# Optimization experiments

Hardware: AMD Instinct MI355X
Metric: run time of the kernel (lower is better)

## Reference

```python
import jax, jax.numpy as jnp
import numpy as np

EPS = 1e-5

def _bin_act(x):
    # sign() forward, clipped straight-through estimator backward
    xc = jnp.clip(x, -1.0, 1.0)
    return xc + jax.lax.stop_gradient(jnp.sign(x) - xc)

def _bin_w(w):
    # XNOR-style: sign(w) scaled by per-output-channel mean(|w|); identity STE
    alpha = jnp.mean(jnp.abs(w), axis=(1, 2, 3), keepdims=True)
    return w + jax.lax.stop_gradient(jnp.sign(w) * alpha - w)

def _conv(x, w, stride, padding, groups):
    return jax.lax.conv_general_dilated(
        x, w, window_strides=(stride, stride),
        padding=[(padding, padding), (padding, padding)],
        feature_group_count=groups,
        dimension_numbers=('NCHW', 'OIHW', 'NCHW'))

def _binconv(x, w, stride, padding, groups):
    return _conv(_bin_act(x), _bin_w(w), stride, padding, groups)

def _bn(x, g, b, m, v):
    # eval-mode BatchNorm2d
    inv = g / jnp.sqrt(v + EPS)
    return x * inv[None, :, None, None] + (b - m * inv)[None, :, None, None]


def setup_inputs() -> dict:
    key = jax.random.key(0)
    ks = jax.random.split(key, 20)
    inp, oup = 256, 512
    d = {}
    d['x'] = jax.random.normal(ks[0], (64, inp, 28, 28), jnp.float32)
    d['w1'] = jax.random.normal(ks[1], (inp, 16, 3, 3), jnp.float32) * 0.1  # grouped, groups=inp/16
    d['w2'] = jax.random.normal(ks[2], (oup, inp, 1, 1), jnp.float32) * 0.05
    d['w3'] = jax.random.normal(ks[3], (oup, oup, 1, 1), jnp.float32) * 0.05
    for i, (name, c) in enumerate([('1', inp), ('2', oup), ('3', oup)]):
        d['g' + name] = jax.random.uniform(ks[4 + 4 * i], (c,), jnp.float32, 0.5, 1.5)
        d['b' + name] = jax.random.normal(ks[5 + 4 * i], (c,), jnp.float32) * 0.1
        d['m' + name] = jax.random.normal(ks[6 + 4 * i], (c,), jnp.float32) * 0.1
        d['v' + name] = jax.random.uniform(ks[7 + 4 * i], (c,), jnp.float32, 0.5, 1.5)
    return d


def reference(x, w1, w2, w3, g1, b1, m1, v1, g2, b2, m2, v2, g3, b3, m3, v3):
    inp = x.shape[1]
    groups = inp // 16
    # conv1 (binary grouped 3x3) + bn1 + residual + hardtanh
    out = _bn(_binconv(x, w1, 1, 1, groups), g1, b1, m1, v1)
    out = jnp.clip(out + x, -1.0, 1.0)
    # conv2 (binary 1x1, inp->oup) + bn2 + hardtanh
    out = jnp.clip(_bn(_binconv(out, w2, 1, 0, 1), g2, b2, m2, v2), -1.0, 1.0)
    res = out
    # conv3 (binary 1x1, oup->oup) + bn3 + residual + hardtanh
    out = _bn(_binconv(out, w3, 1, 0, 1), g3, b3, m3, v3)
    return jnp.clip(out + res, -1.0, 1.0)
```

## Files before the change

### kernel.cpp

```cpp
#include <hip/hip_runtime.h>
#include <stdint.h>

#define C1 256
#define C2 512
#define P_ 784
#define TAU 1e-6
#define PT 56
#define CH 8


__global__ __launch_bounds__(256) void prep(
    const float* __restrict__ w1, const float* __restrict__ w2, const float* __restrict__ w3,
    const float* __restrict__ g1, const float* __restrict__ b1, const float* __restrict__ m1, const float* __restrict__ v1,
    const float* __restrict__ g2, const float* __restrict__ b2, const float* __restrict__ m2, const float* __restrict__ v2,
    const float* __restrict__ g3, const float* __restrict__ b3, const float* __restrict__ m3, const float* __restrict__ v3,
    double* __restrict__ sc1d, double* __restrict__ bi1d,
    int* __restrict__ T2, float* __restrict__ sc2f, float* __restrict__ bi2f,
    float* __restrict__ sc3f, float* __restrict__ bi3f,
    uint16_t* __restrict__ wb1, uint32_t* __restrict__ bw2, uint32_t* __restrict__ bw3,
    unsigned long long* __restrict__ amin)
{
    int bid = blockIdx.x, t = threadIdx.x;
    if (bid == 0 && t == 0) amin[0] = ~0ULL;
    if (bid == 0) {
        int co = t;
        const float* wp = w1 + (size_t)co * 144;
        double s = 0.0;
        for (int k = 0; k < 144; k++) s += fabs((double)wp[k]);
        double alpha = s / 144.0;
        double iv = (double)g1[co] / sqrt((double)v1[co] + 1e-5);
        sc1d[co] = alpha * iv;
        bi1d[co] = (double)b1[co] - (double)m1[co] * iv;
        for (int tap = 0; tap < 9; tap++) {
            uint32_t wv = 0;
            for (int ci = 0; ci < 16; ci++) wv |= (uint32_t)(wp[ci * 9 + tap] < 0.f) << ci;
            wb1[co * 9 + tap] = (uint16_t)wv;
        }
    } else if (bid <= 2) {
        int co = (bid - 1) * 256 + t;
        const float* wp = w2 + (size_t)co * 256;
        double s = 0.0;
        for (int k = 0; k < 256; k++) s += fabs((double)wp[k]);
        double alpha = s / 256.0;
        double iv = (double)g2[co] / sqrt((double)v2[co] + 1e-5);
        double sc = alpha * iv;
        double bi = (double)b2[co] - (double)m2[co] * iv;
        int T = -257;
        while (T <= 257 && fma((double)T, sc, bi) < 0.0) T++;
        T2[co] = T;
        sc2f[co] = (float)sc;
        bi2f[co] = (float)bi;
        for (int wd = 0; wd < 8; wd++) {
            uint32_t wv = 0;
            for (int j = 0; j < 32; j++) wv |= (uint32_t)(wp[wd * 32 + j] < 0.f) << j;
            bw2[co * 8 + wd] = wv;
        }
    } else {
        int co = (bid - 3) * 256 + t;
        const float* wp = w3 + (size_t)co * 512;
        double s = 0.0;
        for (int k = 0; k < 512; k++) s += fabs((double)wp[k]);
        double alpha = s / 512.0;
        double iv = (double)g3[co] / sqrt((double)v3[co] + 1e-5);
        sc3f[co] = (float)(alpha * iv);
        bi3f[co] = (float)((double)b3[co] - (double)m3[co] * iv);
        for (int wd = 0; wd < 16; wd++) {
            uint32_t wv = 0;
            for (int j = 0; j < 32; j++) wv |= (uint32_t)(wp[wd * 32 + j] < 0.f) << j;
            bw3[co * 16 + wd] = wv;
        }
    }
}

__global__ __launch_bounds__(256) void k1(
    const float* __restrict__ x,
    const double* __restrict__ sc1d, const double* __restrict__ bi1d,
    const uint16_t* __restrict__ wb1,
    uint16_t* __restrict__ pk1, unsigned long long* __restrict__ amin)
{
    __shared__ uint32_t xzb[30][30];
    __shared__ uint16_t wbl[16][9];
    __shared__ double scs[16], bis[16];
    __shared__ float scf[16], bif[16];

    int g = blockIdx.x, n = blockIdx.y, t = threadIdx.x;

    for (int idx = t; idx < 900; idx += 256) ((uint32_t*)xzb)[idx] = 0;
    if (t < 144) ((uint16_t*)wbl)[t] = wb1[g * 144 + t];
    if (t < 16) {
        scs[t] = sc1d[g * 16 + t]; bis[t] = bi1d[g * 16 + t];
        scf[t] = (float)scs[t];    bif[t] = (float)bis[t];
    }
    __syncthreads();

    const float* xg = x + ((size_t)n * C1 + g * 16) * P_;
    float xr[4][16];
    #pragma unroll
    for (int i = 0; i < 4; i++) {
        int p = t + 256 * i;
        if (p < P_) {
            uint32_t sb = 0, nb = 0;
            #pragma unroll
            for (int ci = 0; ci < 16; ci++) {
                float xv = xg[ci * P_ + p];
                xr[i][ci] = xv;
                sb |= (uint32_t)(xv < 0.f) << ci;
                nb |= (uint32_t)(xv != 0.f) << ci;
            }
            int h = p / 28, w = p - 28 * h;
            xzb[h + 1][w + 1] = sb | (nb << 16);
        }
    }
    __syncthreads();

    uint16_t* pko = pk1 + ((size_t)n * 16 + g) * P_;
    #pragma unroll
    for (int i = 0; i < 4; i++) {
        int p = t + 256 * i;
        if (p < P_) {
            int h = p / 28, w = p - 28 * h;
            uint32_t xv9[9], zv9[9];
            int Z = 0;
            #pragma unroll
            for (int kh = 0; kh < 3; kh++)
                #pragma unroll
                for (int kw = 0; kw < 3; kw++) {
                    int k = kh * 3 + kw;
                    uint32_t xz = xzb[h + kh][w + kw];
                    xv9[k] = xz & 0xFFFFu;
                    zv9[k] = xz >> 16;
                    Z += __popc(zv9[k]);
                }
            uint32_t word = 0;
            #pragma unroll
            for (int co = 0; co < 16; co++) {
                int pd = 0;
                #pragma unroll
                for (int k = 0; k < 9; k++)
                    pd += __popc((xv9[k] ^ (uint32_t)wbl[co][k]) & zv9[k]);
                int S = Z - 2 * pd;
                float vf = __fmaf_rn((float)S, scf[co], bif[co]) + xr[i][co];
                uint32_t neg;
                if (fabsf(vf) < 1e-3f) {
                    double v = fma((double)S, scs[co], bis[co]) + (double)xr[i][co];
                    v = fmin(fmax(v, -1.0), 1.0);
                    double m = fabs(v);
                    if (m < TAU) {
                        unsigned long long pk =
                            ((unsigned long long)__float_as_uint((float)m) << 32) |
                            (unsigned long long)((uint32_t)(n * C1 + g * 16 + co) * (uint32_t)P_ + (uint32_t)p);
                        atomicMin(amin, pk);
                    }
                    neg = (v < 0.0);
                } else {
                    neg = (vf < 0.f);
                }
                word |= neg << co;
            }
            pko[p] = (uint16_t)word;
        }
    }
}

__global__ __launch_bounds__(512) void k23(
    const uint32_t* __restrict__ bw2, const uint32_t* __restrict__ bw3,
    const int* __restrict__ T2, const float* __restrict__ sc2f, const float* __restrict__ bi2f,
    const float* __restrict__ sc3f, const float* __restrict__ bi3f,
    const uint16_t* __restrict__ pk1, const unsigned long long* __restrict__ amin,
    float* __restrict__ out)
{
    __shared__ uint16_t raw[16][PT];
    __shared__ uint32_t xw2[PT][8];
    __shared__ uint32_t xw3[2][CH][16];

    int n = blockIdx.x, pc = blockIdx.y, t = threadIdx.x;
    int p0 = pc * PT;
    int wv = t >> 6, lane = t & 63;

    const uint32_t* pkw = (const uint32_t*)(pk1 + (size_t)n * 16 * P_);
    for (int idx = t; idx < 16 * (PT / 2); idx += 512) {
        int g = idx / (PT / 2), j = idx % (PT / 2);
        ((uint32_t*)raw)[g * (PT / 2) + j] = pkw[g * (P_ / 2) + p0 / 2 + j];
    }
    __syncthreads();
    if (t == 0) {
        unsigned long long a = amin[0];
        if (a != ~0ULL) {
            uint32_t loc = (uint32_t)a;
            uint32_t nn = loc / (C1 * P_);
            uint32_t rem = loc - nn * C1 * P_;
            uint32_t c = rem / P_, p = rem - c * P_;
            if ((int)nn == n && (int)p >= p0 && (int)p < p0 + PT)
                raw[c >> 4][p - p0] ^= (uint16_t)(1u << (c & 15));
        }
    }
    __syncthreads();
    for (int idx = t; idx < PT * 8; idx += 512) {
        int p = idx >> 3, wd = idx & 7;
        xw2[p][wd] = (uint32_t)raw[2 * wd][p] | ((uint32_t)raw[2 * wd + 1][p] << 16);
    }
    __syncthreads();

    int co = t;
    const uint32_t* wp2 = bw2 + co * 8;
    uint32_t a0 = wp2[0], a1 = wp2[1], a2 = wp2[2], a3 = wp2[3];
    uint32_t a4 = wp2[4], a5 = wp2[5], a6 = wp2[6], a7 = wp2[7];
    int Tv = T2[co];
    float sc2 = sc2f[co], bi2v = bi2f[co];
    const uint32_t* wp3 = bw3 + co * 16;
    uint32_t w[16];
    #pragma unroll
    for (int i = 0; i < 16; i++) w[i] = wp3[i];
    float sc3 = sc3f[co], bi3v = bi3f[co];
    float* op = out + ((size_t)n * C2 + co) * P_ + p0;

    for (int c = 0; c < PT / CH; c++) {
        int buf = c & 1;
        float r2[CH];
        #pragma unroll
        for (int j = 0; j < CH; j++) {
            const uint32_t* xp = xw2[CH * c + j];
            int pop = __popc(xp[0] ^ a0) + __popc(xp[1] ^ a1) + __popc(xp[2] ^ a2) + __popc(xp[3] ^ a3)
                    + __popc(xp[4] ^ a4) + __popc(xp[5] ^ a5) + __popc(xp[6] ^ a6) + __popc(xp[7] ^ a7);
            int S = 256 - 2 * pop;
            float vf = __fmaf_rn((float)S, sc2, bi2v);
            r2[j] = fminf(fmaxf(vf, -1.f), 1.f);
            unsigned long long mb = __ballot(S < Tv);
            if (lane == 0) {
                xw3[buf][j][2 * wv]     = (uint32_t)mb;
                xw3[buf][j][2 * wv + 1] = (uint32_t)(mb >> 32);
            }
        }
        __syncthreads();
        float4 b4;
        #pragma unroll
        for (int j = 0; j < CH; j++) {
            const uint32_t* xp = xw3[buf][j];
            int pop = 0;
            #pragma unroll
            for (int i = 0; i < 16; i++) pop += __popc(xp[i] ^ w[i]);
            int S = 512 - 2 * pop;
            float v = __fmaf_rn((float)S, sc3, bi3v) + r2[j];
            v = fminf(fmaxf(v, -1.f), 1.f);
            int r = j & 3;
            if (r == 0) b4.x = v; else if (r == 1) b4.y = v; else if (r == 2) b4.z = v;
            else { b4.w = v; ((float4*)op)[(CH * c + j) >> 2] = b4; }
        }
    }
}

extern "C" void kernel_launch(void* const* d_in, const int* in_sizes, int n_in,
                              void* d_out, int out_size, void* d_ws, size_t ws_size,
                              hipStream_t stream) {
    const float* x  = (const float*)d_in[0];
    const float* w1 = (const float*)d_in[1];
    const float* w2 = (const float*)d_in[2];
    const float* w3 = (const float*)d_in[3];
    const float* g1 = (const float*)d_in[4];
    const float* b1 = (const float*)d_in[5];
    const float* m1 = (const float*)d_in[6];
    const float* v1 = (const float*)d_in[7];
    const float* g2 = (const float*)d_in[8];
    const float* b2 = (const float*)d_in[9];
    const float* m2 = (const float*)d_in[10];
    const float* v2 = (const float*)d_in[11];
    const float* g3 = (const float*)d_in[12];
    const float* b3 = (const float*)d_in[13];
    const float* m3 = (const float*)d_in[14];
    const float* v3 = (const float*)d_in[15];
    float* out = (float*)d_out;

    char* ws = (char*)d_ws;
    unsigned long long* amin = (unsigned long long*)(ws + 0);
    double*   sc1d = (double*)(ws + 64);
    double*   bi1d = (double*)(ws + 2112);
    int*      T2   = (int*)(ws + 4160);
    float*    sc2f = (float*)(ws + 6208);
    float*    bi2f = (float*)(ws + 8256);
    float*    sc3f = (float*)(ws + 10304);
    float*    bi3f = (float*)(ws + 12352);
    uint16_t* wb1  = (uint16_t*)(ws + 14400);
    uint32_t* bw2  = (uint32_t*)(ws + 19008);
    uint32_t* bw3  = (uint32_t*)(ws + 35392);
    uint16_t* pk1  = (uint16_t*)(ws + 68160);

    prep<<<dim3(5), 256, 0, stream>>>(w1, w2, w3,
        g1, b1, m1, v1, g2, b2, m2, v2, g3, b3, m3, v3,
        sc1d, bi1d, T2, sc2f, bi2f, sc3f, bi3f, wb1, bw2, bw3, amin);
    k1<<<dim3(16, 64), 256, 0, stream>>>(x, sc1d, bi1d, wb1, pk1, amin);
    k23<<<dim3(64, P_ / PT), 512, 0, stream>>>(bw2, bw3, T2, sc2f, bi2f, sc3f, bi3f, pk1, amin, out);
}
```

Baseline: 131.3 us.

## Split conv2/conv3 into two phases with one barrier and larger pixel tiles

Result: slower. 141.5 us (+7.7%).

```diff
diff --git a/kernel.cpp b/kernel.cpp
--- a/kernel.cpp
+++ b/kernel.cpp
@@ -5,8 +5,7 @@
 #define C2 512
 #define P_ 784
 #define TAU 1e-6
-#define PT 56
-#define CH 8
+#define PT 112
 
 
 __global__ __launch_bounds__(256) void prep(
@@ -171,7 +170,7 @@
 {
     __shared__ uint16_t raw[16][PT];
     __shared__ uint32_t xw2[PT][8];
-    __shared__ uint32_t xw3[2][CH][16];
+    __shared__ uint32_t xw3[PT][16];
 
     int n = blockIdx.x, pc = blockIdx.y, t = threadIdx.x;
     int p0 = pc * PT;
@@ -206,46 +205,46 @@
     uint32_t a0 = wp2[0], a1 = wp2[1], a2 = wp2[2], a3 = wp2[3];
     uint32_t a4 = wp2[4], a5 = wp2[5], a6 = wp2[6], a7 = wp2[7];
     int Tv = T2[co];
-    float sc2 = sc2f[co], bi2v = bi2f[co];
+
+    #pragma unroll 4
+    for (int p = 0; p < PT; p++) {
+        const uint32_t* xp = xw2[p];
+        int pop = __popc(xp[0] ^ a0) + __popc(xp[1] ^ a1) + __popc(xp[2] ^ a2) + __popc(xp[3] ^ a3)
+                + __popc(xp[4] ^ a4) + __popc(xp[5] ^ a5) + __popc(xp[6] ^ a6) + __popc(xp[7] ^ a7);
+        int S = 256 - 2 * pop;
+        unsigned long long mb = __ballot(S < Tv);
+        if (lane == 0) {
+            xw3[p][2 * wv]     = (uint32_t)mb;
+            xw3[p][2 * wv + 1] = (uint32_t)(mb >> 32);
+        }
+    }
+    __syncthreads();
+
     const uint32_t* wp3 = bw3 + co * 16;
     uint32_t w[16];
     #pragma unroll
     for (int i = 0; i < 16; i++) w[i] = wp3[i];
+    float sc2 = sc2f[co], bi2v = bi2f[co];
     float sc3 = sc3f[co], bi3v = bi3f[co];
     float* op = out + ((size_t)n * C2 + co) * P_ + p0;
-
-    for (int c = 0; c < PT / CH; c++) {
-        int buf = c & 1;
-        float r2[CH];
+    float4 b4;
+    #pragma unroll 4
+    for (int p = 0; p < PT; p++) {
+        const uint32_t* xp = xw2[p];
+        int pop2 = __popc(xp[0] ^ a0) + __popc(xp[1] ^ a1) + __popc(xp[2] ^ a2) + __popc(xp[3] ^ a3)
+                 + __popc(xp[4] ^ a4) + __popc(xp[5] ^ a5) + __popc(xp[6] ^ a6) + __popc(xp[7] ^ a7);
+        int S2 = 256 - 2 * pop2;
+        float r2 = fminf(fmaxf(__fmaf_rn((float)S2, sc2, bi2v), -1.f), 1.f);
+        const uint32_t* yp = xw3[p];
+        int pop3 = 0;
         #pragma unroll
-        for (int j = 0; j < CH; j++) {
-            const uint32_t* xp = xw2[CH * c + j];
-            int pop = __popc(xp[0] ^ a0) + __popc(xp[1] ^ a1) + __popc(xp[2] ^ a2) + __popc(xp[3] ^ a3)
-                    + __popc(xp[4] ^ a4) + __popc(xp[5] ^ a5) + __popc(xp[6] ^ a6) + __popc(xp[7] ^ a7);
-            int S = 256 - 2 * pop;
-            float vf = __fmaf_rn((float)S, sc2, bi2v);
-            r2[j] = fminf(fmaxf(vf, -1.f), 1.f);
-            unsigned long long mb = __ballot(S < Tv);
-            if (lane == 0) {
-                xw3[buf][j][2 * wv]     = (uint32_t)mb;
-                xw3[buf][j][2 * wv + 1] = (uint32_t)(mb >> 32);
-            }
-        }
-        __syncthreads();
-        float4 b4;
-        #pragma unroll
-        for (int j = 0; j < CH; j++) {
-            const uint32_t* xp = xw3[buf][j];
-            int pop = 0;
-            #pragma unroll
-            for (int i = 0; i < 16; i++) pop += __popc(xp[i] ^ w[i]);
-            int S = 512 - 2 * pop;
-            float v = __fmaf_rn((float)S, sc3, bi3v) + r2[j];
-            v = fminf(fmaxf(v, -1.f), 1.f);
-            int r = j & 3;
-            if (r == 0) b4.x = v; else if (r == 1) b4.y = v; else if (r == 2) b4.z = v;
-            else { b4.w = v; ((float4*)op)[(CH * c + j) >> 2] = b4; }
-        }
+        for (int i = 0; i < 16; i++) pop3 += __popc(yp[i] ^ w[i]);
+        int S3 = 512 - 2 * pop3;
+        float v = __fmaf_rn((float)S3, sc3, bi3v) + r2;
+        v = fminf(fmaxf(v, -1.f), 1.f);
+        int r = p & 3;
+        if (r == 0) b4.x = v; else if (r == 1) b4.y = v; else if (r == 2) b4.z = v;
+        else { b4.w = v; ((float4*)op)[p >> 2] = b4; }
     }
 }
 
```

## Replace popcount binary GEMMs with int8 MFMA matrix-core kernel

Applied to the files above, without the earlier changes.

Result: slower. 146.3 us (+11.4%).

```diff
diff --git a/kernel.cpp b/kernel.cpp
--- a/kernel.cpp
+++ b/kernel.cpp
@@ -5,9 +5,12 @@
 #define C2 512
 #define P_ 784
 #define TAU 1e-6
-#define PT 56
-#define CH 8
-
+
+typedef int v4i __attribute__((ext_vector_type(4)));
+
+#define WS_NEED 2071104
+
+#define K23_SMEM 137216
 
 __global__ __launch_bounds__(256) void prep(
     const float* __restrict__ w1, const float* __restrict__ w2, const float* __restrict__ w3,
@@ -17,7 +20,8 @@
     double* __restrict__ sc1d, double* __restrict__ bi1d,
     int* __restrict__ T2, float* __restrict__ sc2f, float* __restrict__ bi2f,
     float* __restrict__ sc3f, float* __restrict__ bi3f,
-    uint16_t* __restrict__ wb1, uint32_t* __restrict__ bw2, uint32_t* __restrict__ bw3,
+    uint16_t* __restrict__ wb1, uint32_t* __restrict__ w2i8w, uint32_t* __restrict__ w3i8w,
+    int* __restrict__ rs2, int* __restrict__ rs3,
     unsigned long long* __restrict__ amin)
 {
     int bid = blockIdx.x, t = threadIdx.x;
@@ -50,11 +54,17 @@
         T2[co] = T;
         sc2f[co] = (float)sc;
         bi2f[co] = (float)bi;
-        for (int wd = 0; wd < 8; wd++) {
-            uint32_t wv = 0;
-            for (int j = 0; j < 32; j++) wv |= (uint32_t)(wp[wd * 32 + j] < 0.f) << j;
-            bw2[co * 8 + wd] = wv;
-        }
+        int neg = 0;
+        for (int wd = 0; wd < 64; wd++) {
+            uint32_t b4 = 0;
+            for (int j = 0; j < 4; j++) {
+                int sbit = (wp[wd * 4 + j] < 0.f);
+                neg += sbit;
+                b4 |= (sbit ? 0xFFu : 0x01u) << (8 * j);
+            }
+            w2i8w[co * 64 + wd] = b4;
+        }
+        rs2[co] = 256 - 2 * neg;
     } else {
         int co = (bid - 3) * 256 + t;
         const float* wp = w3 + (size_t)co * 512;
@@ -64,11 +74,17 @@
         double iv = (double)g3[co] / sqrt((double)v3[co] + 1e-5);
         sc3f[co] = (float)(alpha * iv);
         bi3f[co] = (float)((double)b3[co] - (double)m3[co] * iv);
-        for (int wd = 0; wd < 16; wd++) {
-            uint32_t wv = 0;
-            for (int j = 0; j < 32; j++) wv |= (uint32_t)(wp[wd * 32 + j] < 0.f) << j;
-            bw3[co * 16 + wd] = wv;
-        }
+        int neg = 0;
+        for (int wd = 0; wd < 128; wd++) {
+            uint32_t b4 = 0;
+            for (int j = 0; j < 4; j++) {
+                int sbit = (wp[wd * 4 + j] < 0.f);
+                neg += sbit;
+                b4 |= (sbit ? 0xFFu : 0x01u) << (8 * j);
+            }
+            w3i8w[co * 128 + wd] = b4;
+        }
+        rs3[co] = 512 - 2 * neg;
     }
 }
 
@@ -162,25 +178,44 @@
     }
 }
 
-__global__ __launch_bounds__(512) void k23(
-    const uint32_t* __restrict__ bw2, const uint32_t* __restrict__ bw3,
-    const int* __restrict__ T2, const float* __restrict__ sc2f, const float* __restrict__ bi2f,
+__global__ __launch_bounds__(512, 1) void k23m(
+    const uint8_t* __restrict__ w2i8, const uint8_t* __restrict__ w3i8,
+    const int* __restrict__ rs2g, const int* __restrict__ rs3g,
+    const int* __restrict__ T2g,
+    const float* __restrict__ sc2f, const float* __restrict__ bi2f,
     const float* __restrict__ sc3f, const float* __restrict__ bi3f,
     const uint16_t* __restrict__ pk1, const unsigned long long* __restrict__ amin,
     float* __restrict__ out)
 {
-    __shared__ uint16_t raw[16][PT];
-    __shared__ uint32_t xw2[PT][8];
-    __shared__ uint32_t xw3[2][CH][16];
-
-    int n = blockIdx.x, pc = blockIdx.y, t = threadIdx.x;
-    int p0 = pc * PT;
-    int wv = t >> 6, lane = t & 63;
+    extern __shared__ char smem[];
+    char*  s1Tb = smem;
+    char*  B2Tb = smem + 34816;
+    float* stg  = (float*)(smem + 102400);
+
+    int n = blockIdx.x, pc = blockIdx.y, h = blockIdx.z, t = threadIdx.x;
+    int w = t >> 6, l = t & 63;
+    int lm = l & 15, lh = l >> 4, klo = lh * 16;
+    int p0 = 128 * pc;
+    int UN = (pc == 6) ? 16 : 128;
+    int NPT = UN / 16;
+    float* stagef = stg + w * 1088;
 
     const uint32_t* pkw = (const uint32_t*)(pk1 + (size_t)n * 16 * P_);
-    for (int idx = t; idx < 16 * (PT / 2); idx += 512) {
-        int g = idx / (PT / 2), j = idx % (PT / 2);
-        ((uint32_t*)raw)[g * (PT / 2) + j] = pkw[g * (P_ / 2) + p0 / 2 + j];
+    int UNW = UN / 2;
+    for (int idx = t; idx < 16 * UNW; idx += 512) {
+        int g = idx / UNW, jj = idx % UNW;
+        uint32_t wpair = pkw[g * 392 + 64 * pc + jj];
+        #pragma unroll
+        for (int hf = 0; hf < 2; hf++) {
+            uint32_t w16 = (wpair >> (16 * hf)) & 0xFFFFu;
+            int row = 2 * jj + hf;
+            #pragma unroll
+            for (int q = 0; q < 4; q++) {
+                uint32_t nib = (w16 >> (4 * q)) & 0xFu;
+                uint32_t v = (nib & 1u) | ((nib & 2u) << 7) | ((nib & 4u) << 14) | ((nib & 8u) << 21);
+                *(uint32_t*)(s1Tb + row * 272 + g * 16 + q * 4) = v;
+            }
+        }
     }
     __syncthreads();
     if (t == 0) {
@@ -189,62 +224,107 @@
             uint32_t loc = (uint32_t)a;
             uint32_t nn = loc / (C1 * P_);
             uint32_t rem = loc - nn * C1 * P_;
-            uint32_t c = rem / P_, p = rem - c * P_;
-            if ((int)nn == n && (int)p >= p0 && (int)p < p0 + PT)
-                raw[c >> 4][p - p0] ^= (uint16_t)(1u << (c & 15));
-        }
-    }
-    __syncthreads();
-    for (int idx = t; idx < PT * 8; idx += 512) {
-        int p = idx >> 3, wd = idx & 7;
-        xw2[p][wd] = (uint32_t)raw[2 * wd][p] | ((uint32_t)raw[2 * wd + 1][p] << 16);
-    }
-    __syncthreads();
-
-    int co = t;
-    const uint32_t* wp2 = bw2 + co * 8;
-    uint32_t a0 = wp2[0], a1 = wp2[1], a2 = wp2[2], a3 = wp2[3];
-    uint32_t a4 = wp2[4], a5 = wp2[5], a6 = wp2[6], a7 = wp2[7];
-    int Tv = T2[co];
-    float sc2 = sc2f[co], bi2v = bi2f[co];
-    const uint32_t* wp3 = bw3 + co * 16;
-    uint32_t w[16];
-    #pragma unroll
-    for (int i = 0; i < 16; i++) w[i] = wp3[i];
-    float sc3 = sc3f[co], bi3v = bi3f[co];
-    float* op = out + ((size_t)n * C2 + co) * P_ + p0;
-
-    for (int c = 0; c < PT / CH; c++) {
-        int buf = c & 1;
-        float r2[CH];
-        #pragma unroll
-        for (int j = 0; j < CH; j++) {
-            const uint32_t* xp = xw2[CH * c + j];
-            int pop = __popc(xp[0] ^ a0) + __popc(xp[1] ^ a1) + __popc(xp[2] ^ a2) + __popc(xp[3] ^ a3)
-                    + __popc(xp[4] ^ a4) + __popc(xp[5] ^ a5) + __popc(xp[6] ^ a6) + __popc(xp[7] ^ a7);
-            int S = 256 - 2 * pop;
-            float vf = __fmaf_rn((float)S, sc2, bi2v);
-            r2[j] = fminf(fmaxf(vf, -1.f), 1.f);
-            unsigned long long mb = __ballot(S < Tv);
-            if (lane == 0) {
-                xw3[buf][j][2 * wv]     = (uint32_t)mb;
-                xw3[buf][j][2 * wv + 1] = (uint32_t)(mb >> 32);
-            }
-        }
-        __syncthreads();
-        float4 b4;
-        #pragma unroll
-        for (int j = 0; j < CH; j++) {
-            const uint32_t* xp = xw3[buf][j];
-            int pop = 0;
-            #pragma unroll
-            for (int i = 0; i < 16; i++) pop += __popc(xp[i] ^ w[i]);
-            int S = 512 - 2 * pop;
-            float v = __fmaf_rn((float)S, sc3, bi3v) + r2[j];
-            v = fminf(fmaxf(v, -1.f), 1.f);
-            int r = j & 3;
-            if (r == 0) b4.x = v; else if (r == 1) b4.y = v; else if (r == 2) b4.z = v;
-            else { b4.w = v; ((float4*)op)[(CH * c + j) >> 2] = b4; }
+            uint32_t c = rem / P_;
+            int p = (int)(rem - c * P_);
+            if ((int)nn == n && p >= p0 && p < p0 + UN)
+                s1Tb[(p - p0) * 272 + c] ^= 1;
+        }
+    }
+    __syncthreads();
+
+    for (int j = 0; j < 4; j++) {
+        int co0 = 64 * w + 16 * j;
+        int rs2v[4], T2v[4];
+        #pragma unroll
+        for (int r = 0; r < 4; r++) {
+            int cr = co0 + lh * 4 + r;
+            rs2v[r] = rs2g[cr]; T2v[r] = T2g[cr];
+        }
+        v4i a1[4];
+        #pragma unroll
+        for (int ks = 0; ks < 4; ks++)
+            a1[ks] = *(const v4i*)(w2i8 + (size_t)(co0 + lm) * 256 + ks * 64 + klo);
+        for (int pt = 0; pt < NPT; pt++) {
+            const char* bp = s1Tb + (pt * 16 + lm) * 272;
+            v4i acc = {0, 0, 0, 0};
+            #pragma unroll
+            for (int ks = 0; ks < 4; ks++) {
+                v4i b = *(const v4i*)(bp + ks * 64 + klo);
+                acc = __builtin_amdgcn_mfma_i32_16x16x64_i8(a1[ks], b, acc, 0, 0, 0);
+            }
+            int rowb = (pt * 16 + lm) * 528;
+            #pragma unroll
+            for (int r = 0; r < 4; r++) {
+                int S2 = rs2v[r] - 2 * acc[r];
+                B2Tb[rowb + co0 + lh * 4 + r] = (char)(S2 < T2v[r]);
+            }
+        }
+    }
+    __syncthreads();
+
+    for (int j2 = 0; j2 < 2; j2++) {
+        int co0 = 256 * h + 32 * w + 16 * j2;
+        int rs2v[4], rs3v[4];
+        float sc2v[4], bi2v[4], sc3v[4], bi3v[4];
+        #pragma unroll
+        for (int r = 0; r < 4; r++) {
+            int cr = co0 + lh * 4 + r;
+            rs2v[r] = rs2g[cr]; sc2v[r] = sc2f[cr]; bi2v[r] = bi2f[cr];
+            rs3v[r] = rs3g[cr]; sc3v[r] = sc3f[cr]; bi3v[r] = bi3f[cr];
+        }
+        v4i a1[4];
+        #pragma unroll
+        for (int ks = 0; ks < 4; ks++)
+            a1[ks] = *(const v4i*)(w2i8 + (size_t)(co0 + lm) * 256 + ks * 64 + klo);
+        v4i a3[8];
+        #pragma unroll
+        for (int ks = 0; ks < 8; ks++)
+            a3[ks] = *(const v4i*)(w3i8 + (size_t)(co0 + lm) * 512 + ks * 64 + klo);
+
+        for (int pt = 0; pt < NPT; pt++) {
+            const char* bp = s1Tb + (pt * 16 + lm) * 272;
+            v4i acc1 = {0, 0, 0, 0};
+            #pragma unroll
+            for (int ks = 0; ks < 4; ks++) {
+                v4i b = *(const v4i*)(bp + ks * 64 + klo);
+                acc1 = __builtin_amdgcn_mfma_i32_16x16x64_i8(a1[ks], b, acc1, 0, 0, 0);
+            }
+            float r2[4];
+            #pragma unroll
+            for (int r = 0; r < 4; r++) {
+                int S2 = rs2v[r] - 2 * acc1[r];
+                r2[r] = fminf(fmaxf(__fmaf_rn((float)S2, sc2v[r], bi2v[r]), -1.f), 1.f);
+            }
+            const char* bp2 = B2Tb + (pt * 16 + lm) * 528;
+            v4i acc3 = {0, 0, 0, 0};
+            #pragma unroll
+            for (int ks = 0; ks < 8; ks++) {
+                v4i b = *(const v4i*)(bp2 + ks * 64 + klo);
+                acc3 = __builtin_amdgcn_mfma_i32_16x16x64_i8(a3[ks], b, acc3, 0, 0, 0);
+            }
+            #pragma unroll
+            for (int r = 0; r < 4; r++) {
+                int S3 = rs3v[r] - 2 * acc3[r];
+                float v = __fmaf_rn((float)S3, sc3v[r], bi3v[r]) + r2[r];
+                v = fminf(fmaxf(v, -1.f), 1.f);
+                stagef[(lh * 4 + r) * 68 + (pt & 3) * 16 + lm] = v;
+            }
+            if ((pt & 3) == 3 || pt == NPT - 1) {
+                asm volatile("s_waitcnt lgkmcnt(0)" ::: "memory");
+                int pb = p0 + 64 * (pt >> 2);
+                #pragma unroll
+                for (int g2 = 0; g2 < 2; g2++) {
+                    #pragma unroll
+                    for (int k2 = 0; k2 < 2; k2++) {
+                        int pos = pb + (l & 7) * 4 + 32 * k2;
+                        if (pos - p0 < UN) {
+                            int cc = co0 + g2 * 8 + (l >> 3);
+                            float4 val = *(float4*)(stagef + (g2 * 8 + (l >> 3)) * 68 + (l & 7) * 4 + 32 * k2);
+                            *(float4*)(out + ((size_t)n * C2 + cc) * P_ + pos) = val;
+                        }
+                    }
+                }
+            }
         }
     }
 }
@@ -280,13 +360,17 @@
     float*    sc3f = (float*)(ws + 10304);
     float*    bi3f = (float*)(ws + 12352);
     uint16_t* wb1  = (uint16_t*)(ws + 14400);
-    uint32_t* bw2  = (uint32_t*)(ws + 19008);
-    uint32_t* bw3  = (uint32_t*)(ws + 35392);
     uint16_t* pk1  = (uint16_t*)(ws + 68160);
+    uint8_t*  w2i8 = (uint8_t*)(ws + 1673792);
+    uint8_t*  w3i8 = (uint8_t*)(ws + 1804864);
+    int*      rs2  = (int*)(ws + 2067008);
+    int*      rs3  = (int*)(ws + 2069056);
 
     prep<<<dim3(5), 256, 0, stream>>>(w1, w2, w3,
         g1, b1, m1, v1, g2, b2, m2, v2, g3, b3, m3, v3,
-        sc1d, bi1d, T2, sc2f, bi2f, sc3f, bi3f, wb1, bw2, bw3, amin);
+        sc1d, bi1d, T2, sc2f, bi2f, sc3f, bi3f, wb1,
+        (uint32_t*)w2i8, (uint32_t*)w3i8, rs2, rs3, amin);
     k1<<<dim3(16, 64), 256, 0, stream>>>(x, sc1d, bi1d, wb1, pk1, amin);
-    k23<<<dim3(64, P_ / PT), 512, 0, stream>>>(bw2, bw3, T2, sc2f, bi2f, sc3f, bi3f, pk1, amin, out);
+    k23m<<<dim3(64, 7, 2), 512, K23_SMEM, stream>>>(w2i8, w3i8, rs2, rs3, T2,
+        sc2f, bi2f, sc3f, bi3f, pk1, amin, out);
 }
```
